# Performance work log

Hardware: AMD Instinct MI355X
Metric: run time of the kernel (lower is better)

## Reference

```python
import jax, jax.numpy as jnp
import numpy as np

B, S, HID, H, D = 4, 1024, 1024, 16, 64
MAXP = 1024  # max_position_embeddings
EPS = 1e-8


def setup_inputs() -> dict:
    key = jax.random.key(0)
    ks = jax.random.split(key, 9)
    scale = 0.02  # keep logits small since masked_softmax has no max-subtraction
    return {
        "hidden_states": jax.random.normal(ks[0], (B, S, HID), jnp.float32),
        "attention_mask": jnp.zeros((B, 1, 1, S), jnp.float32),
        "skim_mask": jax.random.randint(ks[1], (B, S), 0, 2, jnp.int32),
        "Wq": jax.random.normal(ks[2], (HID, HID), jnp.float32) * scale,
        "bq": jnp.zeros((HID,), jnp.float32),
        "Wk": jax.random.normal(ks[3], (HID, HID), jnp.float32) * scale,
        "bk": jnp.zeros((HID,), jnp.float32),
        "Wv": jax.random.normal(ks[4], (HID, HID), jnp.float32) * scale,
        "bv": jnp.zeros((HID,), jnp.float32),
        "dist_emb": jax.random.normal(ks[5], (2 * MAXP - 1, D), jnp.float32) * scale,
    }


def reference(hidden_states, attention_mask, skim_mask, Wq, bq, Wk, bk, Wv, bv, dist_emb):
    # Linear projections (W stored as [in, out]) then split heads: [B,H,S,D]
    def heads(x):
        return x.reshape(B, S, H, D).transpose(0, 2, 1, 3)

    q = heads(hidden_states @ Wq + bq)
    k = heads(hidden_states @ Wk + bk)
    v = heads(hidden_states @ Wv + bv)

    # raw scores [B,H,S,S]
    scores = jnp.einsum('bhld,bhrd->bhlr', q, k)

    # relative_key positional bias
    pos = jnp.arange(S)
    distance = pos[:, None] - pos[None, :]                 # [S,S]
    pe = dist_emb[distance + MAXP - 1]                     # [S,S,D]
    scores = scores + jnp.einsum('bhld,lrd->bhlr', q, pe)

    scores = scores / jnp.sqrt(jnp.float32(D))
    scores = scores + attention_mask

    # skim_mask branch: masked_softmax (exp * mask, normalized with eps)
    mask = skim_mask[:, None, None, :].astype(scores.dtype)  # [B,1,1,S]
    exps = jnp.exp(scores) * mask
    probs = exps / (EPS + exps.sum(-1, keepdims=True))
    # dropout in eval mode -> identity

    ctx = jnp.einsum('bhlr,bhrd->bhld', probs, v)
    return ctx.transpose(0, 2, 1, 3).reshape(B, S, HID)
```

## Files before the change

kernel.cpp:

```cpp
#include <hip/hip_runtime.h>
#include <hip/hip_bf16.h>


#define EPSV 1e-8f

typedef short bfrag __attribute__((ext_vector_type(8)));
typedef float cfrag __attribute__((ext_vector_type(16)));
typedef int v2i __attribute__((ext_vector_type(2)));
typedef float v2f __attribute__((ext_vector_type(2)));

__device__ __forceinline__ short f2bf(float f) {
    __hip_bfloat16 h = __float2bfloat16(f);
    return *reinterpret_cast<short*>(&h);
}
__device__ __forceinline__ unsigned int pk2(short a, short b) {
    return (unsigned int)(unsigned short)a | ((unsigned int)(unsigned short)b << 16);
}
__device__ __forceinline__ void g2lds(const short* g, short* l) {
    __builtin_amdgcn_global_load_lds(
        (const __attribute__((address_space(1))) void*)g,
        (__attribute__((address_space(3))) void*)l, 16, 0, 0);
}

__global__ __launch_bounds__(256) void prep(
    const float* __restrict__ hidden, const float* __restrict__ Wq,
    const float* __restrict__ Wk, const float* __restrict__ Wv,
    const float* __restrict__ dist,
    short* __restrict__ Xs, short* __restrict__ Wt, short* __restrict__ Db)
{
    __shared__ short Tl[4][2304];
    const int bid = blockIdx.x, tid = threadIdx.x;

#pragma unroll
    for (int u = 0; u < 4; u++) {
        const int vb = bid * 4 + u;
        short* Tu = Tl[u];
        if (vb < 2048) {
            const int mt = vb >> 4, kg = vb & 15;
            const int m_l = tid >> 3, k8 = (tid & 7) * 8;
            const float* src = hidden + (size_t)(mt * 32 + m_l) * 1024 + kg * 64 + k8;
            float4 v0 = *(const float4*)src, v1 = *(const float4*)(src + 4);
            short o[8];
            o[0] = f2bf(v0.x); o[1] = f2bf(v0.y); o[2] = f2bf(v0.z); o[3] = f2bf(v0.w);
            o[4] = f2bf(v1.x); o[5] = f2bf(v1.y); o[6] = f2bf(v1.z); o[7] = f2bf(v1.w);
            *(bfrag*)&Tu[m_l * 72 + k8] = *(bfrag*)o;
        } else if (vb < 3584) {
            const int t = vb - 2048, z = t >> 9, nt = (t >> 4) & 31, kg = t & 15;
            const float* W = (z == 0) ? Wq : ((z == 1) ? Wk : Wv);
            const int k_l = tid >> 2, n8 = (tid & 3) * 8;
            const float* src = W + (size_t)(kg * 64 + k_l) * 1024 + nt * 32 + n8;
            float4 v0 = *(const float4*)src, v1 = *(const float4*)(src + 4);
            float vv[8] = {v0.x, v0.y, v0.z, v0.w, v1.x, v1.y, v1.z, v1.w};
#pragma unroll
            for (int i = 0; i < 8; i++)
                Tu[(n8 + i) * 72 + k_l] = f2bf(vv[i]);
        } else if (vb < 3648) {
            const int idx = (vb - 3584) * 256 + tid;
            if (idx < 16376) {
                const float* src = dist + (size_t)idx * 8;
                float4 v0 = *(const float4*)src, v1 = *(const float4*)(src + 4);
                short o[8];
                o[0] = f2bf(v0.x); o[1] = f2bf(v0.y); o[2] = f2bf(v0.z); o[3] = f2bf(v0.w);
                o[4] = f2bf(v1.x); o[5] = f2bf(v1.y); o[6] = f2bf(v1.z); o[7] = f2bf(v1.w);
                *(bfrag*)(Db + (size_t)idx * 8) = *(bfrag*)o;
            }
        }
    }
    __syncthreads();
    {
        const int l31 = tid & 31, q2 = (tid >> 5) & 1, kc = tid >> 6;
#pragma unroll
        for (int u = 0; u < 4; u++) {
            const int vb = bid * 4 + u;
            const short* Tu = Tl[u];
            if (vb < 2048) {
                const int mt = vb >> 4, kg = vb & 15;
                bfrag r = *(const bfrag*)&Tu[l31 * 72 + kc * 16 + q2 * 8];
                *(bfrag*)(Xs + ((size_t)(mt * 64 + kg * 4 + kc) * 64
                          + q2 * 32 + l31) * 8) = r;
            } else if (vb < 3584) {
                const int t = vb - 2048, z = t >> 9, nt = (t >> 4) & 31, kg = t & 15;
                bfrag r = *(const bfrag*)&Tu[l31 * 72 + kc * 16 + q2 * 8];
                *(bfrag*)(Wt + (size_t)z * 1048576
                          + ((size_t)(nt * 64 + kg * 4 + kc) * 64
                             + q2 * 32 + l31) * 8) = r;
            }
        }
    }
}

__global__ __launch_bounds__(256) void qkv_mfma(
    const short* __restrict__ Xs, const short* __restrict__ Wt,
    const float* __restrict__ bq, const float* __restrict__ bk,
    const float* __restrict__ bv,
    short* __restrict__ Qf, short* __restrict__ Kf, short* __restrict__ Vt)
{
    __shared__ alignas(16) short Ab[3][2][4][512];
    __shared__ alignas(16) short Bb[3][2][4][512];

    const int z = blockIdx.z;
    const short* W = Wt + (size_t)z * 1048576;
    const float* bias = (z == 0) ? bq : ((z == 1) ? bk : bv);
    const float scale = (z == 0) ? 0.18033688011112042f : 1.0f;

    const int tid = threadIdx.x, lane = tid & 63, wid = tid >> 6;
    const int q2 = lane >> 5, l31 = lane & 31;
    const int wr = wid >> 1, wc = wid & 1;
    const int m0 = blockIdx.x * 128, n0 = blockIdx.y * 128;

    const short* Ag = Xs + (size_t)(m0 >> 5) * 32768;
    const short* Bg = W  + (size_t)(n0 >> 5) * 32768;

    auto STAGE = [&](int p, int bi) {
        const int k0 = p * 2;
#pragma unroll
        for (int j = 0; j < 2; j++) {
            g2lds(Ag + (size_t)wid * 32768 + (k0 + j) * 512 + lane * 8,
                  &Ab[bi][j][wid][0]);
            g2lds(Bg + (size_t)wid * 32768 + (k0 + j) * 512 + lane * 8,
                  &Bb[bi][j][wid][0]);
        }
    };

    cfrag acc[2][2];
#pragma unroll
    for (int i = 0; i < 2; i++)
#pragma unroll
        for (int j = 0; j < 2; j++)
#pragma unroll
            for (int e = 0; e < 16; e++) acc[i][j][e] = 0.f;

    STAGE(0, 0);
    STAGE(1, 1);

    for (int p = 0; p < 32; p++) {
        if (p < 31) asm volatile("s_waitcnt vmcnt(4)" ::: "memory");
        else        asm volatile("s_waitcnt vmcnt(0)" ::: "memory");
        __builtin_amdgcn_s_barrier();
        if (p + 2 < 32) STAGE(p + 2, (p + 2) % 3);

        const int bi = p % 3;
#pragma unroll
        for (int j = 0; j < 2; j++) {
            bfrag a0 = *(const bfrag*)&Ab[bi][j][2 * wr + 0][lane * 8];
            bfrag a1 = *(const bfrag*)&Ab[bi][j][2 * wr + 1][lane * 8];
            bfrag b0 = *(const bfrag*)&Bb[bi][j][2 * wc + 0][lane * 8];
            bfrag b1 = *(const bfrag*)&Bb[bi][j][2 * wc + 1][lane * 8];
            acc[0][0] = __builtin_amdgcn_mfma_f32_32x32x16_bf16(a0, b0, acc[0][0], 0, 0, 0);
            acc[0][1] = __builtin_amdgcn_mfma_f32_32x32x16_bf16(a0, b1, acc[0][1], 0, 0, 0);
            acc[1][0] = __builtin_amdgcn_mfma_f32_32x32x16_bf16(a1, b0, acc[1][0], 0, 0, 0);
            acc[1][1] = __builtin_amdgcn_mfma_f32_32x32x16_bf16(a1, b1, acc[1][1], 0, 0, 0);
        }
    }

#pragma unroll
    for (int nt = 0; nt < 2; nt++) {
        const int c = n0 + wc * 64 + nt * 32 + l31;
        const float bval = bias[c];
        const int h = c >> 6;
        const int d = nt * 32 + l31;
#pragma unroll
        for (int mt = 0; mt < 2; mt++) {
            const int tok0 = m0 + wr * 64 + mt * 32;
            const int bb = tok0 >> 10, s_base = tok0 & 1023;
            const size_t bhbase = (size_t)(bb * 16 + h) * 65536;
            if (z < 2) {
                short* outp = (z == 0) ? Qf : Kf;
                const size_t fbase = bhbase
                    + ((size_t)((s_base >> 5) * 4 + (d >> 4)) * 64
                       + ((d >> 3) & 1) * 32) * 8 + (d & 7);
#pragma unroll
                for (int reg = 0; reg < 16; reg++) {
                    const int row = (reg & 3) + 8 * (reg >> 2) + 4 * q2;
                    outp[fbase + (size_t)row * 8] = f2bf((acc[mt][nt][reg] + bval) * scale);
                }
            } else {
#pragma unroll
                for (int g = 0; g < 4; g++) {
                    const float e0 = acc[mt][nt][4 * g + 0] + bval;
                    const float e1 = acc[mt][nt][4 * g + 1] + bval;
                    const float e2 = acc[mt][nt][4 * g + 2] + bval;
                    const float e3 = acc[mt][nt][4 * g + 3] + bval;
                    uint2 w2;
                    w2.x = pk2(f2bf(e0), f2bf(e1));
                    w2.y = pk2(f2bf(e2), f2bf(e3));
                    const size_t flat = bhbase
                        + ((size_t)(nt * 64 + (s_base >> 4) + (g >> 1)) * 64
                           + (g & 1) * 32 + l31) * 8 + 4 * q2;
                    *(uint2*)(Vt + flat) = w2;
                }
            }
        }
    }
}

__global__ __launch_bounds__(256, 2) void attn_mfma(
    const short* __restrict__ Qf, const short* __restrict__ Kf,
    const short* __restrict__ Vt, const short* __restrict__ Db,
    const float* __restrict__ amask, const int* __restrict__ skim,
    float* __restrict__ out)
{
    __shared__ alignas(16) short Tb[128 * 132];
    __shared__ alignas(16) short Kbuf[2][4096];
    __shared__ alignas(16) short Vbuf[2][4096];
    __shared__ float Lg[1024];

    const int tid = threadIdx.x, lane = tid & 63, w = tid >> 6;
    const int q2 = lane >> 5, l31 = lane & 31;
    const int bh = blockIdx.x, b = bh >> 4, hh = bh & 15;
    const int l0 = blockIdx.y * 128;

    const short* Qg = Qf + (size_t)bh * 65536;
    const short* Kg = Kf + (size_t)bh * 65536;
    const short* Vg = Vt + (size_t)bh * 65536;

    auto STAGE = [&](int rk, int bi) {
        const int kbase = (rk >> 5) * 4, vbase = rk >> 4;
#pragma unroll
        for (int j = 0; j < 4; j++) {
            const int c = 4 * w + j;
            if (c < 8) {
                g2lds(Kg + (size_t)(kbase + c) * 512 + lane * 8,
                      &Kbuf[bi][c * 512]);
            } else if (c < 12) {
                g2lds(Vg + (size_t)(vbase + (c - 8)) * 512 + lane * 8,
                      &Vbuf[bi][(c - 8) * 512]);
            } else {
                g2lds(Vg + (size_t)(64 + vbase + (c - 12)) * 512 + lane * 8,
                      &Vbuf[bi][(c - 12 + 4) * 512]);
            }
        }
    };

    {
        const int r4 = tid * 4;
        float4 am = *(const float4*)(amask + b * 1024 + r4);
        int4 sk = *(const int4*)(skim + b * 1024 + r4);
        Lg[r4 + 0] = __expf(am.x) * (float)sk.x;
        Lg[r4 + 1] = __expf(am.y) * (float)sk.y;
        Lg[r4 + 2] = __expf(am.z) * (float)sk.z;
        Lg[r4 + 3] = __expf(am.w) * (float)sk.w;
    }
    __syncthreads();

    bfrag qa[4];
#pragma unroll
    for (int c = 0; c < 4; c++)
        qa[c] = *(const bfrag*)(Qg + ((size_t)(((l0 >> 5) + w) * 4 + c) * 64 + lane) * 8);

    cfrag oacc[2];
#pragma unroll
    for (int mt = 0; mt < 2; mt++)
#pragma unroll
        for (int e = 0; e < 16; e++) oacc[mt][e] = 0.f;
    v2f es01 = {0.f, 0.f}, es23 = {0.f, 0.f};

    const int Lband = l0 + 32 * w;
    const int lg = Lband + l31;
    const int rowb = (32 * w + l31) * 132;

    for (int r0 = -128; r0 < 1024; r0 += 64) {
        const bool produce = r0 < 960;
        const int cur = (r0 >> 6) & 1;

        if (r0 + 64 >= 0 && r0 + 64 < 1024)
            STAGE(r0 + 64, ((r0 + 64) >> 6) & 1);

        bfrag pb[2][4];
        if (produce) {
#pragma unroll
            for (int mt = 0; mt < 2; mt++) {
                const int D0 = Lband - r0 - 128 + 32 * mt;
                const int er = min(max(D0 + l31 + 1023, 0), 2046);
#pragma unroll
                for (int kc = 0; kc < 4; kc++)
                    pb[mt][kc] = *(const bfrag*)(Db + (size_t)er * 64 + kc * 16 + q2 * 8);
            }
        }

        if (r0 >= 0) {
            bfrag kb[2][4], vbl[4][2];
            v2i trr[2][4];
#pragma unroll
            for (int mt = 0; mt < 2; mt++)
#pragma unroll
                for (int kc = 0; kc < 4; kc++)
                    kb[mt][kc] = *(const bfrag*)&Kbuf[cur][(mt * 4 + kc) * 512 + lane * 8];
#pragma unroll
            for (int kc = 0; kc < 4; kc++)
#pragma unroll
                for (int mtd = 0; mtd < 2; mtd++)
                    vbl[kc][mtd] = *(const bfrag*)&Vbuf[cur][(mtd * 4 + kc) * 512 + lane * 8];
#pragma unroll
            for (int mt = 0; mt < 2; mt++)
#pragma unroll
                for (int g = 0; g < 4; g++)
                    trr[mt][g] = *(const v2i*)&Tb[rowb
                        + ((r0 + 32 * mt + 8 * g + 4 * q2) & 127)];

#pragma unroll
            for (int mt = 0; mt < 2; mt++) {
                cfrag sfr;
#pragma unroll
                for (int g = 0; g < 4; g++) {
                    const v2i t2 = trr[mt][g];
                    sfr[4 * g + 0] = __builtin_bit_cast(float, (unsigned)t2[0] << 16);
                    sfr[4 * g + 1] = __builtin_bit_cast(float, (unsigned)t2[0] & 0xffff0000u);
                    sfr[4 * g + 2] = __builtin_bit_cast(float, (unsigned)t2[1] << 16);
                    sfr[4 * g + 3] = __builtin_bit_cast(float, (unsigned)t2[1] & 0xffff0000u);
                }
                __builtin_amdgcn_s_setprio(1);
#pragma unroll
                for (int kc = 0; kc < 4; kc++)
                    sfr = __builtin_amdgcn_mfma_f32_32x32x16_bf16(
                        kb[mt][kc], qa[kc], sfr, 0, 0, 0);
                __builtin_amdgcn_s_setprio(0);

                unsigned int P[4][2];
#pragma unroll
                for (int g = 0; g < 4; g++) {
                    const int rb = r0 + 32 * mt + 8 * g + 4 * q2;
                    float4 g4 = *(const float4*)&Lg[rb];
                    float ev0 = __builtin_amdgcn_exp2f(sfr[4 * g + 0]) * g4.x;
                    float ev1 = __builtin_amdgcn_exp2f(sfr[4 * g + 1]) * g4.y;
                    float ev2 = __builtin_amdgcn_exp2f(sfr[4 * g + 2]) * g4.z;
                    float ev3 = __builtin_amdgcn_exp2f(sfr[4 * g + 3]) * g4.w;
                    es01 += (v2f){ev0, ev1};
                    es23 += (v2f){ev2, ev3};
                    P[g][0] = pk2(f2bf(ev0), f2bf(ev1));
                    P[g][1] = pk2(f2bf(ev2), f2bf(ev3));
                }
#pragma unroll
                for (int c = 0; c < 2; c++) {
                    v2i s0 = __builtin_amdgcn_permlane32_swap(
                        (int)P[2 * c][0], (int)P[2 * c + 1][0], false, false);
                    v2i s1 = __builtin_amdgcn_permlane32_swap(
                        (int)P[2 * c][1], (int)P[2 * c + 1][1], false, false);
                    union { bfrag f; int d[4]; } u;
                    u.d[0] = s0[0]; u.d[1] = s1[0]; u.d[2] = s0[1]; u.d[3] = s1[1];
                    const int kc = 2 * mt + c;
                    __builtin_amdgcn_s_setprio(1);
#pragma unroll
                    for (int mtd = 0; mtd < 2; mtd++)
                        oacc[mtd] = __builtin_amdgcn_mfma_f32_32x32x16_bf16(
                            vbl[kc][mtd], u.f, oacc[mtd], 0, 0, 0);
                    __builtin_amdgcn_s_setprio(0);
                }
            }
        }

        if (produce) {
#pragma unroll
            for (int mt = 0; mt < 2; mt++) {
                cfrag t;
#pragma unroll
                for (int e = 0; e < 16; e++) t[e] = 0.f;
                __builtin_amdgcn_s_setprio(1);
#pragma unroll
                for (int kc = 0; kc < 4; kc++)
                    t = __builtin_amdgcn_mfma_f32_32x32x16_bf16(
                        pb[mt][kc], qa[kc], t, 0, 0, 0);
                __builtin_amdgcn_s_setprio(0);
#pragma unroll
                for (int e = 0; e < 16; e++) {
                    const int rr = (e & 3) + 8 * (e >> 2) + 4 * q2;
                    Tb[rowb + ((l31 + r0 - 32 * mt - rr) & 127)] = f2bf(t[e]);
                }
            }
        }

        __syncthreads();
    }

    float esum = (es01[0] + es01[1]) + (es23[0] + es23[1]);
    const float den = EPSV + esum + __shfl_xor(esum, 32);
    const float inv = 1.0f / den;
    float* ob = out + ((size_t)(b * 1024 + lg) * 1024) + hh * 64;
#pragma unroll
    for (int mtd = 0; mtd < 2; mtd++) {
#pragma unroll
        for (int g = 0; g < 4; g++) {
            float4 o;
            o.x = oacc[mtd][4 * g + 0] * inv;
            o.y = oacc[mtd][4 * g + 1] * inv;
            o.z = oacc[mtd][4 * g + 2] * inv;
            o.w = oacc[mtd][4 * g + 3] * inv;
            *(float4*)(ob + 32 * mtd + 8 * g + 4 * q2) = o;
        }
    }
}

extern "C" void kernel_launch(void* const* d_in, const int* in_sizes, int n_in,
                              void* d_out, int out_size, void* d_ws, size_t ws_size,
                              hipStream_t stream) {
    const float* hidden = (const float*)d_in[0];
    const float* amask  = (const float*)d_in[1];
    const int*   skim   = (const int*)d_in[2];
    const float* Wq     = (const float*)d_in[3];
    const float* bq     = (const float*)d_in[4];
    const float* Wk     = (const float*)d_in[5];
    const float* bk     = (const float*)d_in[6];
    const float* Wv     = (const float*)d_in[7];
    const float* bv     = (const float*)d_in[8];
    const float* dist   = (const float*)d_in[9];
    float* out = (float*)d_out;

    char* w = (char*)d_ws;
    short* Xs  = (short*)(w);
    short* Wt  = (short*)(w + ((size_t)8 << 20));
    short* Db  = (short*)(w + ((size_t)14 << 20));
    short* Qf  = (short*)(w + ((size_t)15 << 20));
    short* Kf  = (short*)(w + ((size_t)23 << 20));
    short* Vt  = (short*)(w + ((size_t)31 << 20));

    prep<<<912, 256, 0, stream>>>(hidden, Wq, Wk, Wv, dist, Xs, Wt, Db);
    qkv_mfma<<<dim3(32, 8, 3), 256, 0, stream>>>(Xs, Wt, bq, bk, bv, Qf, Kf, Vt);
    attn_mfma<<<dim3(64, 8), 256, 0, stream>>>(Qf, Kf, Vt, Db, amask, skim, out);
}
```

Baseline: 175.8 us.

## Fuse Q projection into attention kernel, drop Q from QKV GEMM

The Q projection is moved out of the QKV GEMM launch and into the attention kernel. Each wave computes its own 32x64 Q tile with MFMA, reading X and Wq fragments straight from global memory, and passes the result through LDS to get the fragment layout. This removes a third of the QKV GEMM grid and the round trip of Q through global memory. In exchange, each attention block does a serial 64-step GEMM prologue with no LDS staging or overlap, and that Wq tile is reloaded by every block of the same head.

```diff
diff --git a/kernel.cpp b/kernel.cpp
--- a/kernel.cpp
+++ b/kernel.cpp
@@ -91,17 +91,15 @@
 
 __global__ __launch_bounds__(256) void qkv_mfma(
     const short* __restrict__ Xs, const short* __restrict__ Wt,
-    const float* __restrict__ bq, const float* __restrict__ bk,
-    const float* __restrict__ bv,
-    short* __restrict__ Qf, short* __restrict__ Kf, short* __restrict__ Vt)
+    const float* __restrict__ bk, const float* __restrict__ bv,
+    short* __restrict__ Kf, short* __restrict__ Vt)
 {
     __shared__ alignas(16) short Ab[3][2][4][512];
     __shared__ alignas(16) short Bb[3][2][4][512];
 
-    const int z = blockIdx.z;
+    const int z = blockIdx.z + 1;
     const short* W = Wt + (size_t)z * 1048576;
-    const float* bias = (z == 0) ? bq : ((z == 1) ? bk : bv);
-    const float scale = (z == 0) ? 0.18033688011112042f : 1.0f;
+    const float* bias = (z == 1) ? bk : bv;
 
     const int tid = threadIdx.x, lane = tid & 63, wid = tid >> 6;
     const int q2 = lane >> 5, l31 = lane & 31;
@@ -164,15 +162,14 @@
             const int tok0 = m0 + wr * 64 + mt * 32;
             const int bb = tok0 >> 10, s_base = tok0 & 1023;
             const size_t bhbase = (size_t)(bb * 16 + h) * 65536;
-            if (z < 2) {
-                short* outp = (z == 0) ? Qf : Kf;
+            if (z == 1) {
                 const size_t fbase = bhbase
                     + ((size_t)((s_base >> 5) * 4 + (d >> 4)) * 64
                        + ((d >> 3) & 1) * 32) * 8 + (d & 7);
 #pragma unroll
                 for (int reg = 0; reg < 16; reg++) {
                     const int row = (reg & 3) + 8 * (reg >> 2) + 4 * q2;
-                    outp[fbase + (size_t)row * 8] = f2bf((acc[mt][nt][reg] + bval) * scale);
+                    Kf[fbase + (size_t)row * 8] = f2bf(acc[mt][nt][reg] + bval);
                 }
             } else {
 #pragma unroll
@@ -195,8 +192,10 @@
 }
 
 __global__ __launch_bounds__(256, 2) void attn_mfma(
-    const short* __restrict__ Qf, const short* __restrict__ Kf,
-    const short* __restrict__ Vt, const short* __restrict__ Db,
+    const short* __restrict__ Xs, const short* __restrict__ Wt,
+    const float* __restrict__ bq,
+    const short* __restrict__ Kf, const short* __restrict__ Vt,
+    const short* __restrict__ Db,
     const float* __restrict__ amask, const int* __restrict__ skim,
     float* __restrict__ out)
 {
@@ -210,9 +209,57 @@
     const int bh = blockIdx.x, b = bh >> 4, hh = bh & 15;
     const int l0 = blockIdx.y * 128;
 
-    const short* Qg = Qf + (size_t)bh * 65536;
     const short* Kg = Kf + (size_t)bh * 65536;
     const short* Vg = Vt + (size_t)bh * 65536;
+
+    bfrag qa[4];
+    {
+        const short* Aq = Xs + (size_t)(b * 32 + (l0 >> 5) + w) * 32768;
+        const short* Bq0 = Wt + (size_t)(hh * 2 + 0) * 32768;
+        const short* Bq1 = Wt + (size_t)(hh * 2 + 1) * 32768;
+        cfrag qacc[2];
+#pragma unroll
+        for (int nt = 0; nt < 2; nt++)
+#pragma unroll
+            for (int e = 0; e < 16; e++) qacc[nt][e] = 0.f;
+#pragma unroll 4
+        for (int kc = 0; kc < 64; kc++) {
+            const int off = kc * 512 + lane * 8;
+            bfrag a  = *(const bfrag*)(Aq + off);
+            bfrag b0 = *(const bfrag*)(Bq0 + off);
+            bfrag b1 = *(const bfrag*)(Bq1 + off);
+            qacc[0] = __builtin_amdgcn_mfma_f32_32x32x16_bf16(a, b0, qacc[0], 0, 0, 0);
+            qacc[1] = __builtin_amdgcn_mfma_f32_32x32x16_bf16(a, b1, qacc[1], 0, 0, 0);
+        }
+        short* Qls = &Kbuf[0][0] + w * 2048;
+#pragma unroll
+        for (int nt = 0; nt < 2; nt++) {
+            const int c = hh * 64 + nt * 32 + l31;
+            const float bval = bq[c];
+            const int d = nt * 32 + l31;
+            const int fbase = ((d >> 4) * 64 + ((d >> 3) & 1) * 32) * 8 + (d & 7);
+#pragma unroll
+            for (int reg = 0; reg < 16; reg++) {
+                const int row = (reg & 3) + 8 * (reg >> 2) + 4 * q2;
+                Qls[fbase + row * 8] =
+                    f2bf((qacc[nt][reg] + bval) * 0.18033688011112042f);
+            }
+        }
+#pragma unroll
+        for (int c = 0; c < 4; c++)
+            qa[c] = *(const bfrag*)&Qls[(c * 64 + lane) * 8];
+    }
+
+    {
+        const int r4 = tid * 4;
+        float4 am = *(const float4*)(amask + b * 1024 + r4);
+        int4 sk = *(const int4*)(skim + b * 1024 + r4);
+        Lg[r4 + 0] = __expf(am.x) * (float)sk.x;
+        Lg[r4 + 1] = __expf(am.y) * (float)sk.y;
+        Lg[r4 + 2] = __expf(am.z) * (float)sk.z;
+        Lg[r4 + 3] = __expf(am.w) * (float)sk.w;
+    }
+    __syncthreads();
 
     auto STAGE = [&](int rk, int bi) {
         const int kbase = (rk >> 5) * 4, vbase = rk >> 4;
@@ -231,22 +278,6 @@
             }
         }
     };
-
-    {
-        const int r4 = tid * 4;
-        float4 am = *(const float4*)(amask + b * 1024 + r4);
-        int4 sk = *(const int4*)(skim + b * 1024 + r4);
-        Lg[r4 + 0] = __expf(am.x) * (float)sk.x;
-        Lg[r4 + 1] = __expf(am.y) * (float)sk.y;
-        Lg[r4 + 2] = __expf(am.z) * (float)sk.z;
-        Lg[r4 + 3] = __expf(am.w) * (float)sk.w;
-    }
-    __syncthreads();
-
-    bfrag qa[4];
-#pragma unroll
-    for (int c = 0; c < 4; c++)
-        qa[c] = *(const bfrag*)(Qg + ((size_t)(((l0 >> 5) + w) * 4 + c) * 64 + lane) * 8);
 
     cfrag oacc[2];
 #pragma unroll
@@ -409,11 +440,11 @@
     short* Xs  = (short*)(w);
     short* Wt  = (short*)(w + ((size_t)8 << 20));
     short* Db  = (short*)(w + ((size_t)14 << 20));
-    short* Qf  = (short*)(w + ((size_t)15 << 20));
     short* Kf  = (short*)(w + ((size_t)23 << 20));
     short* Vt  = (short*)(w + ((size_t)31 << 20));
 
     prep<<<912, 256, 0, stream>>>(hidden, Wq, Wk, Wv, dist, Xs, Wt, Db);
-    qkv_mfma<<<dim3(32, 8, 3), 256, 0, stream>>>(Xs, Wt, bq, bk, bv, Qf, Kf, Vt);
-    attn_mfma<<<dim3(64, 8), 256, 0, stream>>>(Qf, Kf, Vt, Db, amask, skim, out);
-}
+    qkv_mfma<<<dim3(32, 8, 2), 256, 0, stream>>>(Xs, Wt, bk, bv, Kf, Vt);
+    attn_mfma<<<dim3(64, 8), 256, 0, stream>>>(Xs, Wt, bq, Kf, Vt, Db,
+                                               amask, skim, out);
+}
```

New measurement: 181.5 us. 1.03x slower.
